# Kernel optimization log

Measured on AMD Instinct MI355X. Metric: run time of the kernel, lower is better.

## Reference

```python
import jax, jax.numpy as jnp
import numpy as np
import math

H = 16
D_MODEL = 1024
B, S = 2, 2048

def setup_inputs() -> dict:
    key = jax.random.key(0)
    ks = jax.random.split(key, 7)
    q = jax.random.normal(ks[0], (B, S, D_MODEL), dtype=jnp.float32)
    k = jax.random.normal(ks[1], (B, S, D_MODEL), dtype=jnp.float32)
    v = jax.random.normal(ks[2], (B, S, D_MODEL), dtype=jnp.float32)
    mask = jnp.ones((1, 1, S, S), dtype=jnp.int32)
    sc = 1.0 / math.sqrt(D_MODEL)
    W_Q = jax.random.normal(ks[3], (D_MODEL, D_MODEL), dtype=jnp.float32) * sc
    W_K = jax.random.normal(ks[4], (D_MODEL, D_MODEL), dtype=jnp.float32) * sc
    W_V = jax.random.normal(ks[5], (D_MODEL, D_MODEL), dtype=jnp.float32) * sc
    W_T = jax.random.normal(ks[6], (D_MODEL, D_MODEL), dtype=jnp.float32) * sc
    return {"q": q, "k": k, "v": v, "mask": mask, "W_Q": W_Q, "W_K": W_K, "W_V": W_V, "W_T": W_T}

def reference(q, k, v, mask, W_Q, W_K, W_V, W_T):
    # W matrices stored as (in, out); nn.Linear applies x @ W.T with W (out,in),
    # equivalent here since we treat these directly as projection matrices.
    def split_heads(x):  # [B,S,D] -> [B,H,S,hd]
        Bq, Sq, Dq = x.shape
        return x.reshape(Bq, Sq, H, Dq // H).transpose(0, 2, 1, 3)

    Q = split_heads(q @ W_Q)
    K = split_heads(k @ W_K)
    V = split_heads(v @ W_V)
    d_k = Q.shape[-1]
    score = jnp.einsum("bhqd,bhkd->bhqk", Q, K) / math.sqrt(d_k)
    score = jnp.where(mask == 0, jnp.float32(-1e9), score)
    attn = jax.nn.softmax(score, axis=-1)
    out = jnp.einsum("bhqk,bhkd->bhqd", attn, V)
    out = out.transpose(0, 2, 1, 3).reshape(q.shape[0], q.shape[1], D_MODEL)
    return out @ W_T
```

## Files before the change

### kernel.cpp

```cpp
#include <hip/hip_runtime.h>
#include <hip/hip_bf16.h>
#include <stdint.h>

#define H  16
#define DM 1024
#define BB 2
#define SS 2048
#define HD 64

#define QSCALE 0.18033688011112042f
#define MASKVAL -57.7078f

typedef __attribute__((ext_vector_type(8))) short bf16x8;
typedef __attribute__((ext_vector_type(4))) float f32x4;

__device__ __forceinline__ short f2bf(float f) {
  __hip_bfloat16 h = __float2bfloat16(f);
  return *reinterpret_cast<short*>(&h);
}

__device__ __forceinline__ unsigned pack_bf16(float a, float b) {
#if __has_builtin(__builtin_amdgcn_cvt_pk_bf16_f32)
  typedef __attribute__((ext_vector_type(2))) __bf16 bf16x2_t;
  bf16x2_t p = __builtin_amdgcn_cvt_pk_bf16_f32(a, b);
  unsigned u;
  __builtin_memcpy(&u, &p, 4);
  return u;
#else
  unsigned ua = __builtin_bit_cast(unsigned, a);
  unsigned ub = __builtin_bit_cast(unsigned, b);
  ua = (ua + 0x7FFFu + ((ua >> 16) & 1u)) >> 16;
  ub = (ub + 0x7FFFu + ((ub >> 16) & 1u));
  return (ub & 0xFFFF0000u) | ua;
#endif
}

__device__ __forceinline__ void load16_lds(const short* g, short* l) {
  __builtin_amdgcn_global_load_lds(
      (const __attribute__((address_space(1))) void*)g,
      (__attribute__((address_space(3))) void*)l, 16, 0, 0);
}

__global__ void prep_kernel(const float* __restrict__ Wq, const float* __restrict__ Wk,
                            const float* __restrict__ Wv, const float* __restrict__ Wt,
                            short* __restrict__ WTall,
                            const float* __restrict__ q, const float* __restrict__ k,
                            const float* __restrict__ v, short* __restrict__ Abf,
                            const int4* __restrict__ mask4, int* __restrict__ flag) {
  int z = blockIdx.z;
  int t = threadIdx.x;
  if (z < 4) {
    __shared__ short tile[32][33];
    const float* src = (z == 0) ? Wq : (z == 1) ? Wk : (z == 2) ? Wv : Wt;
    short* out = WTall + (size_t)z * DM * DM;
    int c0 = (blockIdx.x & 31) * 32, r0 = (blockIdx.x >> 5) * 32;
    int tx = t & 31, ty = t >> 5;
    for (int j = 0; j < 4; j++)
      tile[ty + j * 8][tx] = f2bf(src[(size_t)(r0 + ty + j * 8) * DM + c0 + tx]);
    __syncthreads();
    for (int j = 0; j < 4; j++)
      out[(size_t)(c0 + ty + j * 8) * DM + r0 + tx] = tile[tx][ty + j * 8];
  } else if (z < 7) {
    int zz = z - 4;
    const float* src = (zz == 0) ? q : (zz == 1) ? k : v;
    short* out = Abf + (size_t)zz * BB * SS * DM;
#pragma unroll
    for (int j = 0; j < 4; j++) {
      size_t i = ((size_t)blockIdx.x * 1024 + j * 256 + t) * 4;
      float4 f = *(const float4*)&src[i];
      uint2 p = {pack_bf16(f.x, f.y), pack_bf16(f.z, f.w)};
      *(uint2*)&out[i] = p;
    }
  } else {
    int any = 0;
#pragma unroll
    for (int j = 0; j < 4; j++) {
      int idx = blockIdx.x * 1024 + j * 256 + t;
      int4 m = mask4[idx];
      if (m.x == 0 || m.y == 0 || m.z == 0 || m.w == 0) any = 1;
    }
    if (any) atomicOr(flag, 1);
  }
}

__global__ void transpose_w_kernel(const float* __restrict__ Wq, const float* __restrict__ Wk,
                                   const float* __restrict__ Wv, const float* __restrict__ Wt,
                                   short* __restrict__ dst, int* __restrict__ flag) {
  if (blockIdx.x == 0 && blockIdx.y == 0 && blockIdx.z == 0 &&
      threadIdx.y == 0 && threadIdx.x < 2) flag[threadIdx.x] = 0;
  __shared__ short tile[32][33];
  int z = blockIdx.z;
  const float* src = (z == 0) ? Wq : (z == 1) ? Wk : (z == 2) ? Wv : Wt;
  short* out = dst + (size_t)z * DM * DM;
  int c0 = blockIdx.x * 32, r0 = blockIdx.y * 32;
  int tx = threadIdx.x, ty = threadIdx.y;
  for (int j = 0; j < 4; j++)
    tile[ty + j * 8][tx] = f2bf(src[(size_t)(r0 + ty + j * 8) * DM + c0 + tx]);
  __syncthreads();
  for (int j = 0; j < 4; j++)
    out[(size_t)(c0 + ty + j * 8) * DM + r0 + tx] = tile[tx][ty + j * 8];
}

__global__ void mask_scan_kernel(const int4* __restrict__ mask4, int n4, int* __restrict__ flag) {
  int idx = blockIdx.x * blockDim.x + threadIdx.x;
  int stride = gridDim.x * blockDim.x;
  int any = 0;
  for (int i = idx; i < n4; i += stride) {
    int4 m = mask4[i];
    if (m.x == 0 || m.y == 0 || m.z == 0 || m.w == 0) any = 1;
  }
  if (any) atomicOr(flag, 1);
}

__global__ void flag_init_kernel(int* flag) { if (threadIdx.x < 2) flag[threadIdx.x] = 0; }

__global__ void signal_fill_kernel(float* __restrict__ out, int n) {
  int i = blockIdx.x * blockDim.x + threadIdx.x;
  if (i < n) out[i] = 1.0f;
}

template <int AF32>
__device__ __forceinline__ void gemm_fast_body(const void* __restrict__ Av,
                                               const short* __restrict__ Bt,
                                               void* __restrict__ Cv, int mode, float scale,
                                               int m0, int n0) {
  __shared__ __align__(16) short As[128 * 64];
  __shared__ __align__(16) short Bs[128 * 64];
  int t = threadIdx.x;
  int lane = t & 63, w = t >> 6;
  int l16 = lane & 15, quad = lane >> 4;
  int wm = (w >> 1) * 64, wn = (w & 1) * 64;
  f32x4 acc[4][4] = {};

  for (int k0 = 0; k0 < DM; k0 += 64) {
    if (AF32) {
      const float* A = (const float*)Av;
#pragma unroll
      for (int i = 0; i < 8; i++) {
        int c = t + i * 256;
        int row = c >> 4, hseg = c & 15;
        int lseg = (hseg >> 1) ^ (row & 7);
        float4 f = *(const float4*)&A[(size_t)(m0 + row) * DM + k0 + hseg * 4];
        uint2 p = {pack_bf16(f.x, f.y), pack_bf16(f.z, f.w)};
        *(uint2*)&As[row * 64 + lseg * 8 + (hseg & 1) * 4] = p;
      }
    } else {
      const short* A = (const short*)Av;
#pragma unroll
      for (int i = 0; i < 4; i++) {
        int c = t + i * 256;
        int row = c >> 3, seg = c & 7;
        int lseg = seg ^ (row & 7);
        load16_lds(&A[(size_t)(m0 + row) * DM + k0 + lseg * 8], &As[c * 8]);
      }
    }
#pragma unroll
    for (int i = 0; i < 4; i++) {
      int c = t + i * 256;
      int row = c >> 3, seg = c & 7;
      int lseg = seg ^ (row & 7);
      load16_lds(&Bt[(size_t)(n0 + row) * DM + k0 + lseg * 8], &Bs[c * 8]);
    }
    __syncthreads();
#pragma unroll
    for (int h = 0; h < 2; h++) {
      bf16x8 af[4], bfr[4];
#pragma unroll
      for (int i = 0; i < 4; i++)
        af[i] = *(const bf16x8*)&As[(wm + i * 16 + l16) * 64 + (((h * 4 + quad) ^ (l16 & 7)) * 8)];
#pragma unroll
      for (int i = 0; i < 4; i++)
        bfr[i] = *(const bf16x8*)&Bs[(wn + i * 16 + l16) * 64 + (((h * 4 + quad) ^ (l16 & 7)) * 8)];
#pragma unroll
      for (int mi = 0; mi < 4; mi++)
#pragma unroll
        for (int ni = 0; ni < 4; ni++)
          acc[mi][ni] = __builtin_amdgcn_mfma_f32_16x16x32_bf16(af[mi], bfr[ni], acc[mi][ni], 0, 0, 0);
    }
    __syncthreads();
  }

  for (int mi = 0; mi < 4; mi++)
    for (int ni = 0; ni < 4; ni++)
      for (int r = 0; r < 4; r++) {
        int m = m0 + wm + mi * 16 + quad * 4 + r;
        int n = n0 + wn + ni * 16 + l16;
        if (mode == 0) {
          short* C = (short*)Cv;
          int b = m >> 11, s = m & (SS - 1);
          int h = n >> 6, d = n & (HD - 1);
          C[(((size_t)(b * H + h) * SS) + s) * HD + d] = f2bf(acc[mi][ni][r] * scale);
        } else if (mode == 3) {
          short* C = (short*)Cv;
          int h = m >> 6, d = m & (HD - 1);
          int b = n >> 11, s = n & (SS - 1);
          C[((size_t)(b * H + h) * HD + d) * SS + s] = f2bf(acc[mi][ni][r] * scale);
        } else {
          float* C = (float*)Cv;
          C[(size_t)m * DM + n] = acc[mi][ni][r];
        }
      }
}

template <int AF32, int VT>
__global__ __launch_bounds__(256, 2) void gemm_qkv_fast_kernel(
    const void* __restrict__ A0, const void* __restrict__ A1, const void* __restrict__ A2,
    const short* __restrict__ WTall,
    short* __restrict__ Qb, short* __restrict__ Kb, short* __restrict__ Vb) {
  int z = blockIdx.z;
  if (VT && z == 2) {
    gemm_fast_body<0>((const void*)(WTall + 2ull * DM * DM), (const short*)A2, (void*)Vb,
                      3, 1.0f, blockIdx.y * 128, blockIdx.x * 128);
  } else {
    const void* A = (z == 0) ? A0 : (z == 1) ? A1 : A2;
    const short* B = WTall + (size_t)z * DM * DM;
    short* C = (z == 0) ? Qb : (z == 1) ? Kb : Vb;
    gemm_fast_body<AF32>(A, B, (void*)C, 0, (z == 0) ? QSCALE : 1.0f,
                         blockIdx.x * 128, blockIdx.y * 128);
  }
}

__global__ __launch_bounds__(256, 2) void gemm_out_fast_kernel(
    const short* __restrict__ Obuf, const short* __restrict__ WtT, float* __restrict__ out) {
  gemm_fast_body<0>((const void*)Obuf, WtT, (void*)out, 2, 1.0f,
                    blockIdx.x * 128, blockIdx.y * 128);
}

#define LDT 40
#define LDB 136

template <int AF32>
__device__ __forceinline__ void gemm_legacy_body(const void* __restrict__ Av,
                                                 const float* __restrict__ Bm,
                                                 void* __restrict__ Cv, int mode, float scale) {
  __shared__ __align__(16) short As[128 * LDT];
  __shared__ __align__(16) short Bsh[32 * LDB];
  int m0 = blockIdx.x * 128, n0 = blockIdx.y * 128;
  int t = threadIdx.x;
  int lane = t & 63, w = t >> 6;
  int l16 = lane & 15, quad = lane >> 4;
  int wm = (w >> 1) * 64, wn = (w & 1) * 64;
  f32x4 acc[4][4] = {};

  for (int k0 = 0; k0 < DM; k0 += 32) {
    if (AF32) {
      const float* A = (const float*)Av;
      for (int i = 0; i < 4; i++) {
        int c = t + i * 256;
        int row = c >> 3, seg = c & 7;
        float4 f = *(const float4*)&A[(size_t)(m0 + row) * DM + k0 + seg * 4];
        uint2 p = {pack_bf16(f.x, f.y), pack_bf16(f.z, f.w)};
        *(uint2*)&As[row * LDT + seg * 4] = p;
      }
    } else {
      const short* A = (const short*)Av;
      for (int i = 0; i < 2; i++) {
        int c = t + i * 256;
        int row = c >> 2, seg = c & 3;
        *(int4*)&As[row * LDT + seg * 8] = *(const int4*)&A[(size_t)(m0 + row) * DM + k0 + seg * 8];
      }
    }
    for (int i = 0; i < 4; i++) {
      int c = t + i * 256;
      int krow = c >> 5, nseg = c & 31;
      float4 f = *(const float4*)&Bm[(size_t)(k0 + krow) * DM + n0 + nseg * 4];
      uint2 p = {pack_bf16(f.x, f.y), pack_bf16(f.z, f.w)};
      *(uint2*)&Bsh[krow * LDB + nseg * 4] = p;
    }
    __syncthreads();
    bf16x8 af[4], bfr[4];
    for (int i = 0; i < 4; i++) af[i] = *(const bf16x8*)&As[(wm + i * 16 + l16) * LDT + quad * 8];
    for (int i = 0; i < 4; i++) {
      bf16x8 tmp;
      for (int j = 0; j < 8; j++) tmp[j] = Bsh[(quad * 8 + j) * LDB + wn + i * 16 + l16];
      bfr[i] = tmp;
    }
    for (int mi = 0; mi < 4; mi++)
      for (int ni = 0; ni < 4; ni++)
        acc[mi][ni] = __builtin_amdgcn_mfma_f32_16x16x32_bf16(af[mi], bfr[ni], acc[mi][ni], 0, 0, 0);
    __syncthreads();
  }

  for (int mi = 0; mi < 4; mi++)
    for (int ni = 0; ni < 4; ni++)
      for (int r = 0; r < 4; r++) {
        int m = m0 + wm + mi * 16 + quad * 4 + r;
        int n = n0 + wn + ni * 16 + l16;
        if (mode == 0) {
          short* C = (short*)Cv;
          int b = m >> 11, s = m & (SS - 1);
          int h = n >> 6, d = n & (HD - 1);
          C[(((size_t)(b * H + h) * SS) + s) * HD + d] = f2bf(acc[mi][ni][r] * scale);
        } else {
          float* C = (float*)Cv;
          C[(size_t)m * DM + n] = acc[mi][ni][r];
        }
      }
}

__global__ __launch_bounds__(256, 2) void gemm_qkv_legacy_kernel(
    const float* __restrict__ q, const float* __restrict__ k, const float* __restrict__ v,
    const float* __restrict__ B0, const float* __restrict__ B1, const float* __restrict__ B2,
    short* __restrict__ Qb, short* __restrict__ Kb, short* __restrict__ Vb) {
  int z = blockIdx.z;
  const float* A = (z == 0) ? q : (z == 1) ? k : v;
  const float* B = (z == 0) ? B0 : (z == 1) ? B1 : B2;
  short* C = (z == 0) ? Qb : (z == 1) ? Kb : Vb;
  gemm_legacy_body<1>((const void*)A, B, (void*)C, 0, (z == 0) ? QSCALE : 1.0f);
}

__global__ __launch_bounds__(256, 2) void gemm_out_legacy_kernel(
    const short* __restrict__ Obuf, const float* __restrict__ Wt, float* __restrict__ out) {
  gemm_legacy_body<0>((const void*)Obuf, Wt, (void*)out, 2, 1.0f);
}

#define LDP 72

template <int UM>
__device__ __forceinline__ void attn_tile(
    const short* __restrict__ Ksb, const short* __restrict__ Vsb,
    short* __restrict__ Psw, const bf16x8 aq[2], f32x4 oacc[4], float& lsum,
    const int* __restrict__ mask, int qg, int kb) {
  int lane = threadIdx.x & 63;
  int l16 = lane & 15, quad = lane >> 4;

#pragma unroll
  for (int kb2 = 0; kb2 < 4; kb2++) {
    int krow = kb2 * 16 + l16;
    bf16x8 k0 = *(const bf16x8*)&Ksb[krow * 64 + ((quad ^ (l16 & 7)) * 8)];
    bf16x8 k1 = *(const bf16x8*)&Ksb[krow * 64 + (((quad + 4) ^ (l16 & 7)) * 8)];
    f32x4 sc = {};
    __builtin_amdgcn_s_setprio(1);
    sc = __builtin_amdgcn_mfma_f32_16x16x32_bf16(k0, aq[0], sc, 0, 0, 0);
    sc = __builtin_amdgcn_mfma_f32_16x16x32_bf16(k1, aq[1], sc, 0, 0, 0);
    __builtin_amdgcn_s_setprio(0);
    if (UM) {
#pragma unroll
      for (int r = 0; r < 4; r++) {
        int kg = kb + kb2 * 16 + quad * 4 + r;
        if (mask[(size_t)qg * SS + kg] == 0) sc[r] = MASKVAL;
      }
    }
    float p0 = __builtin_exp2f(sc[0]);
    float p1 = __builtin_exp2f(sc[1]);
    float p2 = __builtin_exp2f(sc[2]);
    float p3 = __builtin_exp2f(sc[3]);
    lsum += (p0 + p1) + (p2 + p3);
    uint2 packed = {pack_bf16(p0, p1), pack_bf16(p2, p3)};
    *(uint2*)&Psw[l16 * LDP + kb2 * 16 + quad * 4] = packed;
  }

  __builtin_amdgcn_s_setprio(1);
#pragma unroll
  for (int c = 0; c < 2; c++) {
    bf16x8 ap = *(const bf16x8*)&Psw[l16 * LDP + c * 32 + quad * 8];
#pragma unroll
    for (int nb2 = 0; nb2 < 4; nb2++) {
      bf16x8 bv = *(const bf16x8*)&Vsb[(nb2 * 16 + l16) * 64 + (((c * 4 + quad) ^ (l16 & 7)) * 8)];
      oacc[nb2] = __builtin_amdgcn_mfma_f32_16x16x32_bf16(ap, bv, oacc[nb2], 0, 0, 0);
    }
  }
  __builtin_amdgcn_s_setprio(0);
}

__global__ __launch_bounds__(512, 4) void attn128_kernel(
    const short* __restrict__ Q, const short* __restrict__ K,
    const short* __restrict__ Vt, const int* __restrict__ mask,
    const int* __restrict__ flag, short* __restrict__ O) {
  __shared__ __align__(16) short Ks[2][64 * 64];
  __shared__ __align__(16) short Vs[2][64 * 64];
  __shared__ __align__(16) short Ps[8][16 * LDP];

  int bx = blockIdx.x, by = blockIdx.y;
  int bh = (bx & 7) * 4 + (by >> 3);
  int qt = (by & 7) * 2 + (bx >> 3);
  int q0 = qt * 128;

  int t = threadIdx.x, lane = t & 63, w = t >> 6;
  int l16 = lane & 15, quad = lane >> 4;
  int use_mask = flag[0];

  const short* qrow = Q + ((size_t)bh * SS + q0 + w * 16 + l16) * HD;
  bf16x8 aq[2] = {*(const bf16x8*)&qrow[quad * 8], *(const bf16x8*)&qrow[32 + quad * 8]};

  float lsum = 0.f;
  f32x4 oacc[4] = {};

  const short* Kbase = K  + (size_t)bh * SS * HD;
  const short* Vbase = Vt + (size_t)bh * HD * SS;

  int rp = t >> 3, lc = (t & 7) ^ (rp & 7);
  const short* kSrc = &Kbase[(size_t)rp * HD + lc * 8];
  const short* vSrc = &Vbase[(size_t)rp * SS + lc * 8];
  int qg = q0 + w * 16 + l16;

  load16_lds(kSrc, &Ks[0][t * 8]);
  load16_lds(vSrc, &Vs[0][t * 8]);
  asm volatile("s_waitcnt vmcnt(0)" ::: "memory");
  __builtin_amdgcn_s_barrier();

  int cur = 0;
  if (!use_mask) {
    for (int kt = 0; kt < SS / 64 - 1; kt++) {
      int kb1 = (kt + 1) * 64;
      load16_lds(kSrc + (size_t)kb1 * HD, &Ks[cur ^ 1][t * 8]);
      load16_lds(vSrc + kb1, &Vs[cur ^ 1][t * 8]);
      attn_tile<0>(Ks[cur], Vs[cur], Ps[w], aq, oacc, lsum, mask, qg, kt * 64);
      asm volatile("s_waitcnt vmcnt(0)" ::: "memory");
      __builtin_amdgcn_s_barrier();
      cur ^= 1;
    }
    attn_tile<0>(Ks[cur], Vs[cur], Ps[w], aq, oacc, lsum, mask, qg, SS - 64);
  } else {
    for (int kt = 0; kt < SS / 64 - 1; kt++) {
      int kb1 = (kt + 1) * 64;
      load16_lds(kSrc + (size_t)kb1 * HD, &Ks[cur ^ 1][t * 8]);
      load16_lds(vSrc + kb1, &Vs[cur ^ 1][t * 8]);
      attn_tile<1>(Ks[cur], Vs[cur], Ps[w], aq, oacc, lsum, mask, qg, kt * 64);
      asm volatile("s_waitcnt vmcnt(0)" ::: "memory");
      __builtin_amdgcn_s_barrier();
      cur ^= 1;
    }
    attn_tile<1>(Ks[cur], Vs[cur], Ps[w], aq, oacc, lsum, mask, qg, SS - 64);
  }

  lsum += __shfl_xor(lsum, 16);
  lsum += __shfl_xor(lsum, 32);

  int b = bh >> 4, h = bh & 15;
#pragma unroll
  for (int r = 0; r < 4; r++) {
    float inv = 1.0f / __shfl(lsum, quad * 4 + r);
    int qq = q0 + w * 16 + quad * 4 + r;
#pragma unroll
    for (int nb2 = 0; nb2 < 4; nb2++) {
      int d = nb2 * 16 + l16;
      O[((size_t)(b * SS + qq)) * DM + h * HD + d] = f2bf(oacc[nb2][r] * inv);
    }
  }
}

__global__ __launch_bounds__(256, 4) void attn64_kernel(
    const short* __restrict__ Q, const short* __restrict__ K,
    const short* __restrict__ V, const int* __restrict__ mask,
    const int* __restrict__ flag, short* __restrict__ O) {
  __shared__ __align__(16) short Ks[64 * 64];
  __shared__ __align__(16) short Vs[64 * 64];
  __shared__ __align__(16) short Ps[4][16 * LDP];

  int bh = blockIdx.y;
  int q0 = blockIdx.x * 64;
  int t = threadIdx.x, lane = t & 63, w = t >> 6;
  int l16 = lane & 15, quad = lane >> 4;
  int use_mask = flag[0];

  const short* qrow = Q + ((size_t)bh * SS + q0 + w * 16 + l16) * HD;
  bf16x8 aq0 = *(const bf16x8*)&qrow[quad * 8];
  bf16x8 aq1 = *(const bf16x8*)&qrow[32 + quad * 8];

  float lsum[4] = {0.f, 0.f, 0.f, 0.f};
  f32x4 oacc[4] = {};

  const short* Kbase = K + (size_t)bh * SS * HD;
  const short* Vbase = V + (size_t)bh * SS * HD;
  int dd = t & 63, h2 = t >> 6;

  for (int kt = 0; kt < SS / 64; kt++) {
    int kb = kt * 64;
    for (int i = 0; i < 2; i++) {
      int p = t + i * 256;
      int rp = p >> 3, cp = p & 7;
      int lc = cp ^ (rp & 7);
      load16_lds(&Kbase[(size_t)(kb + rp) * HD + lc * 8], &Ks[p * 8]);
    }
    for (int sgi = 0; sgi < 2; sgi++) {
      int sg = h2 * 2 + sgi;
      short tmp[8];
      for (int jj = 0; jj < 8; jj++)
        tmp[jj] = Vbase[(size_t)(kb + sg * 8 + jj) * HD + dd];
      *(int4*)&Vs[dd * 64 + ((sg ^ (dd & 7)) * 8)] = *(const int4*)tmp;
    }
    __syncthreads();

    for (int nb = 0; nb < 4; nb++) {
      f32x4 sc = {};
      bf16x8 bk0 = *(const bf16x8*)&Ks[(nb * 16 + l16) * 64 + ((quad ^ (l16 & 7)) * 8)];
      bf16x8 bk1 = *(const bf16x8*)&Ks[(nb * 16 + l16) * 64 + (((quad + 4) ^ (l16 & 7)) * 8)];
      sc = __builtin_amdgcn_mfma_f32_16x16x32_bf16(aq0, bk0, sc, 0, 0, 0);
      sc = __builtin_amdgcn_mfma_f32_16x16x32_bf16(aq1, bk1, sc, 0, 0, 0);
      if (use_mask) {
        int kg = kb + nb * 16 + l16;
        for (int r = 0; r < 4; r++) {
          int qg = q0 + w * 16 + quad * 4 + r;
          if (mask[(size_t)qg * SS + kg] == 0) sc[r] = MASKVAL;
        }
      }
      for (int r = 0; r < 4; r++) {
        float pv = __builtin_exp2f(sc[r]);
        lsum[r] += pv;
        Ps[w][(quad * 4 + r) * LDP + nb * 16 + l16] = f2bf(pv);
      }
    }

    for (int c = 0; c < 2; c++) {
      bf16x8 ap = *(const bf16x8*)&Ps[w][l16 * LDP + c * 32 + quad * 8];
      for (int nb2 = 0; nb2 < 4; nb2++) {
        bf16x8 bv = *(const bf16x8*)&Vs[(nb2 * 16 + l16) * 64 + (((c * 4 + quad) ^ (l16 & 7)) * 8)];
        oacc[nb2] = __builtin_amdgcn_mfma_f32_16x16x32_bf16(ap, bv, oacc[nb2], 0, 0, 0);
      }
    }
    __syncthreads();
  }

  for (int st = 1; st < 16; st <<= 1)
    for (int r = 0; r < 4; r++) lsum[r] += __shfl_xor(lsum[r], st);

  int b = bh >> 4, h = bh & 15;
  for (int r = 0; r < 4; r++) {
    float inv = 1.0f / lsum[r];
    int qg = q0 + w * 16 + quad * 4 + r;
    for (int nb2 = 0; nb2 < 4; nb2++) {
      int d = nb2 * 16 + l16;
      O[((size_t)(b * SS + qg)) * DM + h * HD + d] = f2bf(oacc[nb2][r] * inv);
    }
  }
}

extern "C" void kernel_launch(void* const* d_in, const int* in_sizes, int n_in,
                              void* d_out, int out_size, void* d_ws, size_t ws_size,
                              hipStream_t stream) {
  const float* q    = (const float*)d_in[0];
  const float* k    = (const float*)d_in[1];
  const float* v    = (const float*)d_in[2];
  const int*   mask = (const int*)d_in[3];
  const float* Wq   = (const float*)d_in[4];
  const float* Wk   = (const float*)d_in[5];
  const float* Wv   = (const float*)d_in[6];
  const float* Wt   = (const float*)d_in[7];
  float* out = (float*)d_out;

  char* ws = (char*)d_ws;
  const size_t MB = 1024ull * 1024ull;
  const size_t NEED_A = 66 * MB;
  const size_t NEED_B = 40 * MB + 4096;
  const size_t NEED_C = 32 * MB + 4096;

  if (ws_size >= NEED_A) {
    short* WTall = (short*)(ws);
    short* Qbuf  = (short*)(ws + 8 * MB);
    short* Kbuf  = (short*)(ws + 16 * MB);
    short* Vtbuf = (short*)(ws + 24 * MB);
    short* Obuf  = (short*)(ws + 32 * MB);
    int*   flag  = (int*)(ws + 40 * MB);
    short* Abf   = (short*)(ws + 41 * MB);

    hipMemsetAsync(flag, 0, 8, stream);
    prep_kernel<<<dim3(1024, 1, 8), 256, 0, stream>>>(
        Wq, Wk, Wv, Wt, WTall, q, k, v, Abf, (const int4*)mask, flag);
    gemm_qkv_fast_kernel<0, 1><<<dim3(BB * SS / 128, DM / 128, 3), 256, 0, stream>>>(
        Abf, Abf + (size_t)BB * SS * DM, Abf + 2ull * BB * SS * DM, WTall, Qbuf, Kbuf, Vtbuf);
    attn128_kernel<<<dim3(SS / 128, BB * H), 512, 0, stream>>>(Qbuf, Kbuf, Vtbuf, mask, flag, Obuf);
    gemm_out_fast_kernel<<<dim3(BB * SS / 128, DM / 128), 256, 0, stream>>>(
        Obuf, WTall + 3ull * DM * DM, out);
  } else if (ws_size >= NEED_B) {
    short* WTall = (short*)(ws);
    short* Qbuf  = (short*)(ws + 8 * MB);
    short* Kbuf  = (short*)(ws + 16 * MB);
    short* Vbuf  = (short*)(ws + 24 * MB);
    short* Obuf  = (short*)(ws + 32 * MB);
    int*   flag  = (int*)(ws + 40 * MB);

    transpose_w_kernel<<<dim3(32, 32, 4), dim3(32, 8), 0, stream>>>(Wq, Wk, Wv, Wt, WTall, flag);
    mask_scan_kernel<<<512, 256, 0, stream>>>((const int4*)mask, SS * SS / 4, flag);
    gemm_qkv_fast_kernel<1, 0><<<dim3(BB * SS / 128, DM / 128, 3), 256, 0, stream>>>(
        q, k, v, WTall, Qbuf, Kbuf, Vbuf);
    attn64_kernel<<<dim3(SS / 64, BB * H), 256, 0, stream>>>(Qbuf, Kbuf, Vbuf, mask, flag, Obuf);
    gemm_out_fast_kernel<<<dim3(BB * SS / 128, DM / 128), 256, 0, stream>>>(
        Obuf, WTall + 3ull * DM * DM, out);
  } else if (ws_size >= NEED_C) {
    short* Qbuf = (short*)(ws);
    short* Kbuf = (short*)(ws + 8 * MB);
    short* Vbuf = (short*)(ws + 16 * MB);
    short* Obuf = (short*)(ws + 24 * MB);
    int*   flag = (int*)(ws + 32 * MB);

    flag_init_kernel<<<1, 64, 0, stream>>>(flag);
    mask_scan_kernel<<<512, 256, 0, stream>>>((const int4*)mask, SS * SS / 4, flag);
    gemm_qkv_legacy_kernel<<<dim3(BB * SS / 128, DM / 128, 3), 256, 0, stream>>>(
        q, k, v, Wq, Wk, Wv, Qbuf, Kbuf, Vbuf);
    attn64_kernel<<<dim3(SS / 64, BB * H), 256, 0, stream>>>(Qbuf, Kbuf, Vbuf, mask, flag, Obuf);
    gemm_out_legacy_kernel<<<dim3(BB * SS / 128, DM / 128), 256, 0, stream>>>(Obuf, Wt, out);
  } else {
    signal_fill_kernel<<<(BB * SS * DM + 255) / 256, 256, 0, stream>>>(out, BB * SS * DM);
  }
}
```

Baseline: 234.4 us.

## Fuse q/k bf16 conversion into QKV GEMM and shrink output GEMM tile

The prep kernel now converts only v to bf16. q and k are read as fp32 directly inside the QKV GEMM, which removes a separate conversion pass and its extra global traffic at the cost of fp32 loads and in-loop packing. The GEMM body gains a BM template parameter, and the output projection uses 64-row tiles so it launches twice as many blocks and fills the GPU better. The setprio hints around the attention score MFMAs are also removed.

```diff
diff --git a/kernel.cpp b/kernel.cpp
--- a/kernel.cpp
+++ b/kernel.cpp
@@ -44,7 +44,6 @@
 __global__ void prep_kernel(const float* __restrict__ Wq, const float* __restrict__ Wk,
                             const float* __restrict__ Wv, const float* __restrict__ Wt,
                             short* __restrict__ WTall,
-                            const float* __restrict__ q, const float* __restrict__ k,
                             const float* __restrict__ v, short* __restrict__ Abf,
                             const int4* __restrict__ mask4, int* __restrict__ flag) {
   int z = blockIdx.z;
@@ -60,16 +59,13 @@
     __syncthreads();
     for (int j = 0; j < 4; j++)
       out[(size_t)(c0 + ty + j * 8) * DM + r0 + tx] = tile[tx][ty + j * 8];
-  } else if (z < 7) {
-    int zz = z - 4;
-    const float* src = (zz == 0) ? q : (zz == 1) ? k : v;
-    short* out = Abf + (size_t)zz * BB * SS * DM;
+  } else if (z == 4) {
 #pragma unroll
     for (int j = 0; j < 4; j++) {
       size_t i = ((size_t)blockIdx.x * 1024 + j * 256 + t) * 4;
-      float4 f = *(const float4*)&src[i];
+      float4 f = *(const float4*)&v[i];
       uint2 p = {pack_bf16(f.x, f.y), pack_bf16(f.z, f.w)};
-      *(uint2*)&out[i] = p;
+      *(uint2*)&Abf[i] = p;
     }
   } else {
     int any = 0;
@@ -119,24 +115,25 @@
   if (i < n) out[i] = 1.0f;
 }
 
-template <int AF32>
+template <int AF32, int BM>
 __device__ __forceinline__ void gemm_fast_body(const void* __restrict__ Av,
                                                const short* __restrict__ Bt,
                                                void* __restrict__ Cv, int mode, float scale,
                                                int m0, int n0) {
-  __shared__ __align__(16) short As[128 * 64];
+  constexpr int MI = BM / 32;
+  __shared__ __align__(16) short As[BM * 64];
   __shared__ __align__(16) short Bs[128 * 64];
   int t = threadIdx.x;
   int lane = t & 63, w = t >> 6;
   int l16 = lane & 15, quad = lane >> 4;
-  int wm = (w >> 1) * 64, wn = (w & 1) * 64;
-  f32x4 acc[4][4] = {};
+  int wm = (w >> 1) * (BM / 2), wn = (w & 1) * 64;
+  f32x4 acc[MI][4] = {};
 
   for (int k0 = 0; k0 < DM; k0 += 64) {
     if (AF32) {
       const float* A = (const float*)Av;
 #pragma unroll
-      for (int i = 0; i < 8; i++) {
+      for (int i = 0; i < 2 * MI; i++) {
         int c = t + i * 256;
         int row = c >> 4, hseg = c & 15;
         int lseg = (hseg >> 1) ^ (row & 7);
@@ -147,7 +144,7 @@
     } else {
       const short* A = (const short*)Av;
 #pragma unroll
-      for (int i = 0; i < 4; i++) {
+      for (int i = 0; i < MI; i++) {
         int c = t + i * 256;
         int row = c >> 3, seg = c & 7;
         int lseg = seg ^ (row & 7);
@@ -164,15 +161,15 @@
     __syncthreads();
 #pragma unroll
     for (int h = 0; h < 2; h++) {
-      bf16x8 af[4], bfr[4];
-#pragma unroll
-      for (int i = 0; i < 4; i++)
+      bf16x8 af[MI], bfr[4];
+#pragma unroll
+      for (int i = 0; i < MI; i++)
         af[i] = *(const bf16x8*)&As[(wm + i * 16 + l16) * 64 + (((h * 4 + quad) ^ (l16 & 7)) * 8)];
 #pragma unroll
       for (int i = 0; i < 4; i++)
         bfr[i] = *(const bf16x8*)&Bs[(wn + i * 16 + l16) * 64 + (((h * 4 + quad) ^ (l16 & 7)) * 8)];
 #pragma unroll
-      for (int mi = 0; mi < 4; mi++)
+      for (int mi = 0; mi < MI; mi++)
 #pragma unroll
         for (int ni = 0; ni < 4; ni++)
           acc[mi][ni] = __builtin_amdgcn_mfma_f32_16x16x32_bf16(af[mi], bfr[ni], acc[mi][ni], 0, 0, 0);
@@ -180,7 +177,7 @@
     __syncthreads();
   }
 
-  for (int mi = 0; mi < 4; mi++)
+  for (int mi = 0; mi < MI; mi++)
     for (int ni = 0; ni < 4; ni++)
       for (int r = 0; r < 4; r++) {
         int m = m0 + wm + mi * 16 + quad * 4 + r;
@@ -202,28 +199,32 @@
       }
 }
 
-template <int AF32, int VT>
+template <int AQK, int VT>
 __global__ __launch_bounds__(256, 2) void gemm_qkv_fast_kernel(
     const void* __restrict__ A0, const void* __restrict__ A1, const void* __restrict__ A2,
     const short* __restrict__ WTall,
     short* __restrict__ Qb, short* __restrict__ Kb, short* __restrict__ Vb) {
   int z = blockIdx.z;
-  if (VT && z == 2) {
-    gemm_fast_body<0>((const void*)(WTall + 2ull * DM * DM), (const short*)A2, (void*)Vb,
-                      3, 1.0f, blockIdx.y * 128, blockIdx.x * 128);
+  if (z == 2) {
+    if (VT) {
+      gemm_fast_body<0, 128>((const void*)(WTall + 2ull * DM * DM), (const short*)A2,
+                             (void*)Vb, 3, 1.0f, blockIdx.y * 128, blockIdx.x * 128);
+    } else {
+      gemm_fast_body<AQK, 128>(A2, WTall + 2ull * DM * DM, (void*)Vb, 0, 1.0f,
+                               blockIdx.x * 128, blockIdx.y * 128);
+    }
   } else {
-    const void* A = (z == 0) ? A0 : (z == 1) ? A1 : A2;
-    const short* B = WTall + (size_t)z * DM * DM;
-    short* C = (z == 0) ? Qb : (z == 1) ? Kb : Vb;
-    gemm_fast_body<AF32>(A, B, (void*)C, 0, (z == 0) ? QSCALE : 1.0f,
-                         blockIdx.x * 128, blockIdx.y * 128);
+    const void* A = (z == 0) ? A0 : A1;
+    gemm_fast_body<AQK, 128>(A, WTall + (size_t)z * DM * DM,
+                             (void*)((z == 0) ? Qb : Kb), 0, (z == 0) ? QSCALE : 1.0f,
+                             blockIdx.x * 128, blockIdx.y * 128);
   }
 }
 
 __global__ __launch_bounds__(256, 2) void gemm_out_fast_kernel(
     const short* __restrict__ Obuf, const short* __restrict__ WtT, float* __restrict__ out) {
-  gemm_fast_body<0>((const void*)Obuf, WtT, (void*)out, 2, 1.0f,
-                    blockIdx.x * 128, blockIdx.y * 128);
+  gemm_fast_body<0, 64>((const void*)Obuf, WtT, (void*)out, 2, 1.0f,
+                        blockIdx.x * 64, blockIdx.y * 128);
 }
 
 #define LDT 40
@@ -330,10 +331,8 @@
     bf16x8 k0 = *(const bf16x8*)&Ksb[krow * 64 + ((quad ^ (l16 & 7)) * 8)];
     bf16x8 k1 = *(const bf16x8*)&Ksb[krow * 64 + (((quad + 4) ^ (l16 & 7)) * 8)];
     f32x4 sc = {};
-    __builtin_amdgcn_s_setprio(1);
     sc = __builtin_amdgcn_mfma_f32_16x16x32_bf16(k0, aq[0], sc, 0, 0, 0);
     sc = __builtin_amdgcn_mfma_f32_16x16x32_bf16(k1, aq[1], sc, 0, 0, 0);
-    __builtin_amdgcn_s_setprio(0);
     if (UM) {
 #pragma unroll
       for (int r = 0; r < 4; r++) {
@@ -555,12 +554,12 @@
     short* Abf   = (short*)(ws + 41 * MB);
 
     hipMemsetAsync(flag, 0, 8, stream);
-    prep_kernel<<<dim3(1024, 1, 8), 256, 0, stream>>>(
-        Wq, Wk, Wv, Wt, WTall, q, k, v, Abf, (const int4*)mask, flag);
-    gemm_qkv_fast_kernel<0, 1><<<dim3(BB * SS / 128, DM / 128, 3), 256, 0, stream>>>(
-        Abf, Abf + (size_t)BB * SS * DM, Abf + 2ull * BB * SS * DM, WTall, Qbuf, Kbuf, Vtbuf);
+    prep_kernel<<<dim3(1024, 1, 6), 256, 0, stream>>>(
+        Wq, Wk, Wv, Wt, WTall, v, Abf, (const int4*)mask, flag);
+    gemm_qkv_fast_kernel<1, 1><<<dim3(BB * SS / 128, DM / 128, 3), 256, 0, stream>>>(
+        q, k, Abf, WTall, Qbuf, Kbuf, Vtbuf);
     attn128_kernel<<<dim3(SS / 128, BB * H), 512, 0, stream>>>(Qbuf, Kbuf, Vtbuf, mask, flag, Obuf);
-    gemm_out_fast_kernel<<<dim3(BB * SS / 128, DM / 128), 256, 0, stream>>>(
+    gemm_out_fast_kernel<<<dim3(BB * SS / 64, DM / 128), 256, 0, stream>>>(
         Obuf, WTall + 3ull * DM * DM, out);
   } else if (ws_size >= NEED_B) {
     short* WTall = (short*)(ws);
@@ -575,7 +574,7 @@
     gemm_qkv_fast_kernel<1, 0><<<dim3(BB * SS / 128, DM / 128, 3), 256, 0, stream>>>(
         q, k, v, WTall, Qbuf, Kbuf, Vbuf);
     attn64_kernel<<<dim3(SS / 64, BB * H), 256, 0, stream>>>(Qbuf, Kbuf, Vbuf, mask, flag, Obuf);
-    gemm_out_fast_kernel<<<dim3(BB * SS / 128, DM / 128), 256, 0, stream>>>(
+    gemm_out_fast_kernel<<<dim3(BB * SS / 64, DM / 128), 256, 0, stream>>>(
         Obuf, WTall + 3ull * DM * DM, out);
   } else if (ws_size >= NEED_C) {
     short* Qbuf = (short*)(ws);
```

Result: slower. 247.8 us (+5.7%).
